# Optimization experiments

Measured on AMD Instinct MI355X. Metric: run time of the kernel, lower is better.

## Reference

```python
import jax, jax.numpy as jnp
import numpy as np

JITTER_EPS = 0.01  # router_jitter_noise


def sparsemixer_top2(scores, jitter_eps):
    # scores: [T, E]. Faithful port of PhiMoE sparsemixer (top_k == 2).
    E = scores.shape[-1]
    eye = jnp.arange(E)
    # ---- expert 1 ----
    max1 = jnp.max(scores, axis=-1, keepdims=True)
    ind1 = jnp.argmax(scores, axis=-1)                      # [T]
    factor1 = jnp.maximum(jnp.abs(scores), max1)            # scores.abs().clamp(min=max)
    mask1 = (max1 - scores) / factor1 > 2.0 * jitter_eps
    gates1 = jax.nn.softmax(jnp.where(mask1, -jnp.inf, scores), axis=-1)
    mult1 = jnp.take_along_axis(gates1, ind1[:, None], axis=-1)   # [T,1]
    # ---- expert 2: mask out first pick, repeat ----
    oh1 = eye[None, :] == ind1[:, None]
    masked_scores = jnp.where(oh1, -jnp.inf, scores)
    max2 = jnp.max(masked_scores, axis=-1, keepdims=True)
    ind2 = jnp.argmax(masked_scores, axis=-1)
    factor2 = jnp.maximum(jnp.abs(scores), max2)
    mask2 = (max2 - scores) / factor2 > 2.0 * jitter_eps
    gates2 = jax.nn.softmax(jnp.where(mask2, -jnp.inf, masked_scores), axis=-1)
    mult2 = jnp.take_along_axis(gates2, ind2[:, None], axis=-1)   # [T,1]
    topk_w = jnp.concatenate([mult1, mult2], axis=-1)       # [T,2]
    topk_ids = jnp.stack([ind1, ind2], axis=-1)             # [T,2]
    return topk_w, topk_ids


def setup_inputs() -> dict:
    key = jax.random.key(0)
    ks = jax.random.split(key, 5)
    B, S, D, F, E = 2, 2048, 1024, 2048, 8
    hidden_states = jax.random.normal(ks[0], (B, S, D), dtype=jnp.float32)
    gate_w = jax.random.normal(ks[1], (E, D), dtype=jnp.float32) * (D ** -0.5)
    w_gate = jax.random.normal(ks[2], (E, F, D), dtype=jnp.float32) * (D ** -0.5)
    w_up = jax.random.normal(ks[3], (E, F, D), dtype=jnp.float32) * (D ** -0.5)
    w_down = jax.random.normal(ks[4], (E, D, F), dtype=jnp.float32) * (F ** -0.5)
    return {"hidden_states": hidden_states, "gate_w": gate_w,
            "w_gate": w_gate, "w_up": w_up, "w_down": w_down}


def reference(hidden_states, gate_w, w_gate, w_up, w_down):
    B, S, D = hidden_states.shape
    E = gate_w.shape[0]
    x = hidden_states.reshape(-1, D)                         # [T,D]
    router_logits = x @ gate_w.T                             # [T,E]
    topk_w, topk_ids = sparsemixer_top2(router_logits, JITTER_EPS)
    # per-token combine weights over experts: [T,E]
    comb = jnp.sum(topk_w[:, :, None] *
                   (topk_ids[:, :, None] == jnp.arange(E)[None, None, :]).astype(topk_w.dtype),
                   axis=1)
    out = jnp.zeros_like(x)
    for e in range(E):  # small fixed expert count
        h = jax.nn.silu(x @ w_gate[e].T) * (x @ w_up[e].T)   # [T,F]
        out = out + comb[:, e:e + 1] * (h @ w_down[e].T)     # [T,D]
    return out.reshape(B, S, D), router_logits
```

## Files before the change

kernel.cpp:

```cpp
#include <hip/hip_runtime.h>
#include <stdint.h>

#define TOK    4096
#define DMODEL 1024
#define FDIM   2048
#define NEXP   8
#define MAXP   10240
#define MAXT   40
#define OUT_MAIN (TOK * DMODEL)

#define IDX_NT  24
#define IDX_TE  32
#define IDX_TR  112

#define OFF_META 0
#define OFF_TKW  33792
#define OFF_PTOK 66560
#define OFF_PW   107520
#define OFF_XG   148480
#define OFF_H    21120000
#define OFF_WGB  63063040
#define OFF_WUB  96617472
#define OFF_WDB  130171904
#define OFF_PV   OFF_WGB
#define OFF_RPOS 163726336
#define WS_NEED  163759104

typedef __attribute__((ext_vector_type(8)))  __bf16 bf16x8;
typedef __attribute__((ext_vector_type(8)))  unsigned short u16x8;
typedef __attribute__((ext_vector_type(4)))  unsigned short u16x4;
typedef __attribute__((ext_vector_type(16))) float f32x16;

__device__ __forceinline__ unsigned short f2bf(float f) {
  unsigned u = __builtin_bit_cast(unsigned, f);
  u += 0x7fffu + ((u >> 16) & 1u);
  return (unsigned short)(u >> 16);
}

__device__ __forceinline__ void async_load16(const void* g, void* l) {
  __builtin_amdgcn_global_load_lds(
      (__attribute__((address_space(1))) void*)g,
      (__attribute__((address_space(3))) void*)l, 16, 0, 0);
}

__device__ __forceinline__ bf16x8 ld_frag(const unsigned short* p) {
  return __builtin_bit_cast(bf16x8, *(const u16x8*)p);
}

__global__ void k_prep(const float* __restrict__ wg, const float* __restrict__ wu,
                       const float* __restrict__ wd, unsigned short* __restrict__ wgb,
                       unsigned short* __restrict__ wub, unsigned short* __restrict__ wdb,
                       const float* __restrict__ x, const float* __restrict__ gw,
                       float* __restrict__ logits, int pre) {
  int b = blockIdx.x;
  if (b < 24576) {
    if (!pre) return;
    const float* src; unsigned short* dst; int bb;
    if (b < 8192)       { src = wg; dst = wgb; bb = b; }
    else if (b < 16384) { src = wu; dst = wub; bb = b - 8192; }
    else                { src = wd; dst = wdb; bb = b - 16384; }
    size_t i = ((size_t)bb * 256 + threadIdx.x) * 8;
    float4 a = *(const float4*)(src + i);
    float4 c = *(const float4*)(src + i + 4);
    u16x8 v = {f2bf(a.x), f2bf(a.y), f2bf(a.z), f2bf(a.w),
               f2bf(c.x), f2bf(c.y), f2bf(c.z), f2bf(c.w)};
    *(u16x8*)(dst + i) = v;
    return;
  }
  int lane = threadIdx.x & 63;
  int t = (b - 24576) * 4 + (threadIdx.x >> 6);
  double acc[NEXP];
#pragma unroll
  for (int e = 0; e < NEXP; ++e) acc[e] = 0.0;
  const float* xp = x + (size_t)t * DMODEL;
  for (int i = 0; i < DMODEL / 64; ++i) {
    int d = i * 64 + lane;
    float xv = xp[d];
#pragma unroll
    for (int e = 0; e < NEXP; ++e) acc[e] += (double)xv * (double)gw[e * DMODEL + d];
  }
#pragma unroll
  for (int e = 0; e < NEXP; ++e) {
    double v = acc[e];
#pragma unroll
    for (int off = 32; off > 0; off >>= 1) v += __shfl_down(v, off, 64);
    if (lane == 0) logits[t * NEXP + e] = (float)v;
  }
}

__global__ __launch_bounds__(1024) void k_route2(
    const float* __restrict__ logits, int* __restrict__ meta,
    float* __restrict__ tk_w, int* __restrict__ ptok, float* __restrict__ pw,
    int* __restrict__ rpos) {
  __shared__ int cnt[NEXP], cur[NEXP], seg[NEXP];
  int tid = threadIdx.x;
  if (tid < NEXP) { cnt[tid] = 0; cur[tid] = 0; }
  for (int r = tid; r < MAXP; r += 1024) ptok[r] = -1;
  __syncthreads();
  int i1[4], i2[4]; float w1v[4], w2v[4];
#pragma unroll
  for (int j = 0; j < 4; ++j) {
    int t = tid + j * 1024;
    float s[NEXP];
#pragma unroll
    for (int e = 0; e < NEXP; ++e) s[e] = logits[t * NEXP + e];
    float max1 = s[0]; int ind1 = 0;
#pragma unroll
    for (int e = 1; e < NEXP; ++e) if (s[e] > max1) { max1 = s[e]; ind1 = e; }
    float sum1 = 0.f;
#pragma unroll
    for (int e = 0; e < NEXP; ++e) {
      float f = fmaxf(fabsf(s[e]), max1);
      if (!((max1 - s[e]) / f > 0.02f)) sum1 += expf(s[e] - max1);
    }
    float max2 = -3.4e38f; int ind2 = 0;
#pragma unroll
    for (int e = 0; e < NEXP; ++e) if (e != ind1 && s[e] > max2) { max2 = s[e]; ind2 = e; }
    float sum2 = 0.f;
#pragma unroll
    for (int e = 0; e < NEXP; ++e) {
      if (e == ind1) continue;
      float f = fmaxf(fabsf(s[e]), max2);
      if (!((max2 - s[e]) / f > 0.02f)) sum2 += expf(s[e] - max2);
    }
    i1[j] = ind1; i2[j] = ind2; w1v[j] = 1.f / sum1; w2v[j] = 1.f / sum2;
    atomicAdd(&cnt[ind1], 1);
    atomicAdd(&cnt[ind2], 1);
  }
  __syncthreads();
  if (tid == 0) {
    int off = 0, nt2 = 0;
    for (int e = 0; e < NEXP; ++e) {
      seg[e] = off;
      int tiles = (cnt[e] + 255) >> 8;
      for (int j = 0; j < tiles; ++j) {
        meta[IDX_TE + nt2] = e;
        meta[IDX_TR + nt2] = off + (j << 8);
        ++nt2;
      }
      off += tiles << 8;
    }
    meta[IDX_NT] = nt2;
  }
  __syncthreads();
#pragma unroll
  for (int j = 0; j < 4; ++j) {
    int t = tid + j * 1024;
    int e1 = i1[j];
    int p1 = atomicAdd(&cur[e1], 1);
    int r1 = seg[e1] + p1;
    ptok[r1] = t; pw[r1] = w1v[j]; rpos[2 * t] = r1; tk_w[2 * t] = w1v[j];
    int e2 = i2[j];
    int p2 = atomicAdd(&cur[e2], 1);
    int r2 = seg[e2] + p2;
    ptok[r2] = t; pw[r2] = w2v[j]; rpos[2 * t + 1] = r2; tk_w[2 * t + 1] = w2v[j];
  }
}

__global__ void k_gather(const float* __restrict__ x, const int* __restrict__ ptok,
                         unsigned short* __restrict__ xg) {
  int r = blockIdx.x;
  int t = ptok[r];
  int c = threadIdx.x << 2;
  unsigned short o0 = 0, o1 = 0, o2 = 0, o3 = 0;
  if (t >= 0) {
    float4 v = *(const float4*)(x + ((size_t)t << 10) + c);
    o0 = f2bf(v.x); o1 = f2bf(v.y); o2 = f2bf(v.z); o3 = f2bf(v.w);
  }
  u16x4 o = {o0, o1, o2, o3};
  *(u16x4*)(xg + ((size_t)r << 10) + c) = o;
}

template <bool PRE>
__global__ __launch_bounds__(512, 2) void k_gu(
    const unsigned short* __restrict__ xg,
    const float* __restrict__ wg32, const float* __restrict__ wu32,
    const unsigned short* __restrict__ wgb, const unsigned short* __restrict__ wub,
    unsigned short* __restrict__ h, const int* __restrict__ meta) {
  int p = blockIdx.x;
  int xcd = p & 7, slot = p >> 3;
  int bx = (slot / 40) * 8 + (slot & 7);
  int rt = xcd * 5 + ((slot % 40) >> 3);

  int nt = meta[IDX_NT];
  if (rt >= nt) return;
  int e = meta[IDX_TE + rt];
  int row0 = meta[IDX_TR + rt];
  int n0 = bx * 128;

  __shared__ __align__(16) unsigned short sA[2][16384];
  __shared__ __align__(16) unsigned short sBg[2][8192];
  __shared__ __align__(16) unsigned short sBu[2][8192];

  int tid = threadIdx.x, lane = tid & 63, w = tid >> 6;
  int wm = w & 1, wn = w >> 1;
  int l31 = lane & 31, lh = lane >> 5;

  f32x16 accg[4], accu[4];
#pragma unroll
  for (int m = 0; m < 4; ++m) {
#pragma unroll
    for (int r = 0; r < 16; ++r) { accg[m][r] = 0.f; accu[m][r] = 0.f; }
  }

  const unsigned short* Abase =
      xg + (size_t)(row0 + w * 32 + l31) * DMODEL + lh * 8;
  int cb0 = w * 2, cb1 = cb0 + 1;
  const unsigned short *G0, *G1, *U0, *U1;
  if constexpr (PRE) {
    const unsigned short* WgB = wgb + (size_t)e * FDIM * DMODEL;
    const unsigned short* WuB = wub + (size_t)e * FDIM * DMODEL;
    size_t o0 = (size_t)(n0 + ((cb0 >> 2) << 5) + l31) * DMODEL + ((cb0 & 3) << 4) + lh * 8;
    size_t o1 = (size_t)(n0 + ((cb1 >> 2) << 5) + l31) * DMODEL + ((cb1 & 3) << 4) + lh * 8;
    G0 = WgB + o0; G1 = WgB + o1; U0 = WuB + o0; U1 = WuB + o1;
  }
  const float* Wg = nullptr; const float* Wu = nullptr;
  if constexpr (!PRE) {
    Wg = wg32 + (size_t)e * FDIM * DMODEL;
    Wu = wu32 + (size_t)e * FDIM * DMODEL;
  }

  auto stage = [&](int buf, int ks) {
    int k0 = ks * 64;
    async_load16(Abase + k0,      &sA[buf][(w * 4 + 0) * 512]);
    async_load16(Abase + k0 + 16, &sA[buf][(w * 4 + 1) * 512]);
    async_load16(Abase + k0 + 32, &sA[buf][(w * 4 + 2) * 512]);
    async_load16(Abase + k0 + 48, &sA[buf][(w * 4 + 3) * 512]);
    if constexpr (PRE) {
      async_load16(G0 + k0, &sBg[buf][cb0 * 512]);
      async_load16(G1 + k0, &sBg[buf][cb1 * 512]);
      async_load16(U0 + k0, &sBu[buf][cb0 * 512]);
      async_load16(U1 + k0, &sBu[buf][cb1 * 512]);
    } else {
#pragma unroll
      for (int i2 = 0; i2 < 2; ++i2) {
        int tau = tid + 512 * i2;
        int c = tau >> 6, l = tau & 63;
        int nrow = n0 + ((c >> 2) << 5) + (l & 31);
        int kk = k0 + ((c & 3) << 4) + ((l >> 5) << 3);
        const float* sg = Wg + (size_t)nrow * DMODEL + kk;
        const float* su = Wu + (size_t)nrow * DMODEL + kk;
        float4 g0 = *(const float4*)sg;
        float4 g1 = *(const float4*)(sg + 4);
        float4 u0 = *(const float4*)su;
        float4 u1 = *(const float4*)(su + 4);
        u16x8 vg = {f2bf(g0.x), f2bf(g0.y), f2bf(g0.z), f2bf(g0.w),
                    f2bf(g1.x), f2bf(g1.y), f2bf(g1.z), f2bf(g1.w)};
        u16x8 vu = {f2bf(u0.x), f2bf(u0.y), f2bf(u0.z), f2bf(u0.w),
                    f2bf(u1.x), f2bf(u1.y), f2bf(u1.z), f2bf(u1.w)};
        *(u16x8*)&sBg[buf][c * 512 + l * 8] = vg;
        *(u16x8*)&sBu[buf][c * 512 + l * 8] = vu;
      }
    }
  };

  auto compute = [&](int buf) {
#pragma unroll
    for (int kq = 0; kq < 4; ++kq) {
      bf16x8 a0 = ld_frag(&sA[buf][((wm * 4 + 0) * 4 + kq) * 512 + lane * 8]);
      bf16x8 a1 = ld_frag(&sA[buf][((wm * 4 + 1) * 4 + kq) * 512 + lane * 8]);
      bf16x8 a2 = ld_frag(&sA[buf][((wm * 4 + 2) * 4 + kq) * 512 + lane * 8]);
      bf16x8 a3 = ld_frag(&sA[buf][((wm * 4 + 3) * 4 + kq) * 512 + lane * 8]);
      bf16x8 vg = ld_frag(&sBg[buf][(wn * 4 + kq) * 512 + lane * 8]);
      bf16x8 vu = ld_frag(&sBu[buf][(wn * 4 + kq) * 512 + lane * 8]);
      accg[0] = __builtin_amdgcn_mfma_f32_32x32x16_bf16(a0, vg, accg[0], 0, 0, 0);
      accg[1] = __builtin_amdgcn_mfma_f32_32x32x16_bf16(a1, vg, accg[1], 0, 0, 0);
      accg[2] = __builtin_amdgcn_mfma_f32_32x32x16_bf16(a2, vg, accg[2], 0, 0, 0);
      accg[3] = __builtin_amdgcn_mfma_f32_32x32x16_bf16(a3, vg, accg[3], 0, 0, 0);
      accu[0] = __builtin_amdgcn_mfma_f32_32x32x16_bf16(a0, vu, accu[0], 0, 0, 0);
      accu[1] = __builtin_amdgcn_mfma_f32_32x32x16_bf16(a1, vu, accu[1], 0, 0, 0);
      accu[2] = __builtin_amdgcn_mfma_f32_32x32x16_bf16(a2, vu, accu[2], 0, 0, 0);
      accu[3] = __builtin_amdgcn_mfma_f32_32x32x16_bf16(a3, vu, accu[3], 0, 0, 0);
    }
  };

  int cur = 0;
  stage(0, 0);
  if constexpr (PRE) {
#pragma unroll 2
    for (int ks = 0; ks < DMODEL / 64; ++ks) {
      if (ks + 1 < DMODEL / 64) {
        stage(cur ^ 1, ks + 1);
        asm volatile("s_waitcnt vmcnt(8)" ::: "memory");
      } else {
        asm volatile("s_waitcnt vmcnt(0)" ::: "memory");
      }
      __builtin_amdgcn_s_barrier();
      __builtin_amdgcn_s_setprio(1);
      compute(cur);
      __builtin_amdgcn_s_setprio(0);
      __builtin_amdgcn_s_barrier();
      cur ^= 1;
    }
  } else {
    __syncthreads();
    for (int ks = 0; ks < DMODEL / 64; ++ks) {
      if (ks + 1 < DMODEL / 64) stage(cur ^ 1, ks + 1);
      compute(cur);
      __syncthreads();
      cur ^= 1;
    }
  }

  int col = n0 + wn * 32 + l31;
#pragma unroll
  for (int m = 0; m < 4; ++m) {
#pragma unroll
    for (int r = 0; r < 16; ++r) {
      int lrow = wm * 128 + m * 32 + (r & 3) + ((r >> 2) << 3) + lh * 4;
      float gv = accg[m][r], uv = accu[m][r];
      float hv = gv * uv / (1.f + __expf(-gv));
      h[(size_t)(row0 + lrow) * FDIM + col] = f2bf(hv);
    }
  }
}

template <bool PRE>
__global__ __launch_bounds__(512, 2) void k_down(
    const unsigned short* __restrict__ h, const float* __restrict__ wd32,
    const unsigned short* __restrict__ wdb, float* __restrict__ out,
    float* __restrict__ pv, const int* __restrict__ meta,
    const int* __restrict__ ptok, const float* __restrict__ pw) {
  int p = blockIdx.x;
  int xcd = p & 7, slot = p >> 3;
  int bx = slot & 7;
  int rt = xcd * 5 + (slot >> 3);

  int nt = meta[IDX_NT];
  if (rt >= nt) return;
  int e = meta[IDX_TE + rt];
  int row0 = meta[IDX_TR + rt];
  int d0 = bx * 128;

  __shared__ __align__(16) unsigned short sA[2][16384];
  __shared__ __align__(16) unsigned short sB[2][8192];
  __shared__ int stok[256];
  __shared__ float sw_[256];

  int tid = threadIdx.x, lane = tid & 63, w = tid >> 6;
  int wm = w & 1, wn = w >> 1;
  int l31 = lane & 31, lh = lane >> 5;

  if constexpr (!PRE) {
    if (tid < 256) { stok[tid] = ptok[row0 + tid]; sw_[tid] = pw[row0 + tid]; }
  }

  f32x16 acc[4];
#pragma unroll
  for (int m = 0; m < 4; ++m) {
#pragma unroll
    for (int r = 0; r < 16; ++r) acc[m][r] = 0.f;
  }

  const unsigned short* Abase =
      h + (size_t)(row0 + w * 32 + l31) * FDIM + lh * 8;
  int cb0 = w * 2, cb1 = cb0 + 1;
  const unsigned short *D0, *D1;
  if constexpr (PRE) {
    const unsigned short* WdB = wdb + (size_t)e * DMODEL * FDIM;
    D0 = WdB + (size_t)(d0 + ((cb0 >> 2) << 5) + l31) * FDIM + ((cb0 & 3) << 4) + lh * 8;
    D1 = WdB + (size_t)(d0 + ((cb1 >> 2) << 5) + l31) * FDIM + ((cb1 & 3) << 4) + lh * 8;
  }
  const float* Wd = nullptr;
  if constexpr (!PRE) Wd = wd32 + (size_t)e * DMODEL * FDIM;

  auto stage = [&](int buf, int ks) {
    int k0 = ks * 64;
    async_load16(Abase + k0,      &sA[buf][(w * 4 + 0) * 512]);
    async_load16(Abase + k0 + 16, &sA[buf][(w * 4 + 1) * 512]);
    async_load16(Abase + k0 + 32, &sA[buf][(w * 4 + 2) * 512]);
    async_load16(Abase + k0 + 48, &sA[buf][(w * 4 + 3) * 512]);
    if constexpr (PRE) {
      async_load16(D0 + k0, &sB[buf][cb0 * 512]);
      async_load16(D1 + k0, &sB[buf][cb1 * 512]);
    } else {
#pragma unroll
      for (int i2 = 0; i2 < 2; ++i2) {
        int tau = tid + 512 * i2;
        int c = tau >> 6, l = tau & 63;
        int drow = d0 + ((c >> 2) << 5) + (l & 31);
        int kk = k0 + ((c & 3) << 4) + ((l >> 5) << 3);
        const float* sd = Wd + (size_t)drow * FDIM + kk;
        float4 b0 = *(const float4*)sd;
        float4 b1 = *(const float4*)(sd + 4);
        u16x8 vb = {f2bf(b0.x), f2bf(b0.y), f2bf(b0.z), f2bf(b0.w),
                    f2bf(b1.x), f2bf(b1.y), f2bf(b1.z), f2bf(b1.w)};
        *(u16x8*)&sB[buf][c * 512 + l * 8] = vb;
      }
    }
  };

  auto compute = [&](int buf) {
#pragma unroll
    for (int kq = 0; kq < 4; ++kq) {
      bf16x8 a0 = ld_frag(&sA[buf][((wm * 4 + 0) * 4 + kq) * 512 + lane * 8]);
      bf16x8 a1 = ld_frag(&sA[buf][((wm * 4 + 1) * 4 + kq) * 512 + lane * 8]);
      bf16x8 a2 = ld_frag(&sA[buf][((wm * 4 + 2) * 4 + kq) * 512 + lane * 8]);
      bf16x8 a3 = ld_frag(&sA[buf][((wm * 4 + 3) * 4 + kq) * 512 + lane * 8]);
      bf16x8 vb = ld_frag(&sB[buf][(wn * 4 + kq) * 512 + lane * 8]);
      acc[0] = __builtin_amdgcn_mfma_f32_32x32x16_bf16(a0, vb, acc[0], 0, 0, 0);
      acc[1] = __builtin_amdgcn_mfma_f32_32x32x16_bf16(a1, vb, acc[1], 0, 0, 0);
      acc[2] = __builtin_amdgcn_mfma_f32_32x32x16_bf16(a2, vb, acc[2], 0, 0, 0);
      acc[3] = __builtin_amdgcn_mfma_f32_32x32x16_bf16(a3, vb, acc[3], 0, 0, 0);
    }
  };

  int cur = 0;
  stage(0, 0);
  if constexpr (PRE) {
#pragma unroll 2
    for (int ks = 0; ks < FDIM / 64; ++ks) {
      if (ks + 1 < FDIM / 64) {
        stage(cur ^ 1, ks + 1);
        asm volatile("s_waitcnt vmcnt(6)" ::: "memory");
      } else {
        asm volatile("s_waitcnt vmcnt(0)" ::: "memory");
      }
      __builtin_amdgcn_s_barrier();
      __builtin_amdgcn_s_setprio(1);
      compute(cur);
      __builtin_amdgcn_s_setprio(0);
      __builtin_amdgcn_s_barrier();
      cur ^= 1;
    }
  } else {
    __syncthreads();
    for (int ks = 0; ks < FDIM / 64; ++ks) {
      if (ks + 1 < FDIM / 64) stage(cur ^ 1, ks + 1);
      compute(cur);
      __syncthreads();
      cur ^= 1;
    }
  }

  int col = d0 + wn * 32 + l31;
#pragma unroll
  for (int m = 0; m < 4; ++m) {
#pragma unroll
    for (int r = 0; r < 16; ++r) {
      int lrow = wm * 128 + m * 32 + (r & 3) + ((r >> 2) << 3) + lh * 4;
      if constexpr (PRE) {
        pv[(size_t)(row0 + lrow) * DMODEL + col] = acc[m][r];
      } else {
        int t = stok[lrow];
        if (t >= 0) atomicAdd(&out[(size_t)t * DMODEL + col], acc[m][r] * sw_[lrow]);
      }
    }
  }
}

__global__ void k_combine(const float* __restrict__ pv, const int* __restrict__ rpos,
                          const float* __restrict__ tkw, float* __restrict__ out) {
  int t = blockIdx.x;
  int r1 = rpos[2 * t], r2 = rpos[2 * t + 1];
  float w1 = tkw[2 * t], w2 = tkw[2 * t + 1];
  int c = threadIdx.x << 2;
  float4 a = *(const float4*)(pv + (size_t)r1 * DMODEL + c);
  float4 b = *(const float4*)(pv + (size_t)r2 * DMODEL + c);
  float4 o;
  o.x = w1 * a.x + w2 * b.x;
  o.y = w1 * a.y + w2 * b.y;
  o.z = w1 * a.z + w2 * b.z;
  o.w = w1 * a.w + w2 * b.w;
  *(float4*)(out + (size_t)t * DMODEL + c) = o;
}

extern "C" void kernel_launch(void* const* d_in, const int* in_sizes, int n_in,
                              void* d_out, int out_size, void* d_ws, size_t ws_size,
                              hipStream_t stream) {
  const float* x  = (const float*)d_in[0];
  const float* gw = (const float*)d_in[1];
  const float* wg = (const float*)d_in[2];
  const float* wu = (const float*)d_in[3];
  const float* wd = (const float*)d_in[4];
  float* out = (float*)d_out;
  float* logits = out + OUT_MAIN;

  char* wsb = (char*)d_ws;
  int* meta = (int*)(wsb + OFF_META);
  float* tk_w = (float*)(wsb + OFF_TKW);
  int* ptok = (int*)(wsb + OFF_PTOK);
  float* pw = (float*)(wsb + OFF_PW);
  unsigned short* xg = (unsigned short*)(wsb + OFF_XG);
  unsigned short* h = (unsigned short*)(wsb + OFF_H);
  unsigned short* wgb = (unsigned short*)(wsb + OFF_WGB);
  unsigned short* wub = (unsigned short*)(wsb + OFF_WUB);
  unsigned short* wdb = (unsigned short*)(wsb + OFF_WDB);
  float* pv = (float*)(wsb + OFF_PV);
  int* rpos = (int*)(wsb + OFF_RPOS);

  bool pre = ws_size >= (size_t)WS_NEED;
  if (!pre) hipMemsetAsync(out, 0, (size_t)OUT_MAIN * sizeof(float), stream);

  k_prep<<<25600, 256, 0, stream>>>(wg, wu, wd, wgb, wub, wdb, x, gw, logits, (int)pre);
  k_route2<<<1, 1024, 0, stream>>>(logits, meta, tk_w, ptok, pw, rpos);
  k_gather<<<MAXP, 256, 0, stream>>>(x, ptok, xg);
  if (pre) {
    k_gu<true><<<(FDIM / 128) * MAXT, 512, 0, stream>>>(xg, wg, wu, wgb, wub, h, meta);
    k_down<true><<<(DMODEL / 128) * MAXT, 512, 0, stream>>>(h, wd, wdb, out, pv, meta, ptok, pw);
    k_combine<<<TOK, 256, 0, stream>>>(pv, rpos, tk_w, out);
  } else {
    k_gu<false><<<(FDIM / 128) * MAXT, 512, 0, stream>>>(xg, wg, wu, wgb, wub, h, meta);
    k_down<false><<<(DMODEL / 128) * MAXT, 512, 0, stream>>>(h, wd, wdb, out, pv, meta, ptok, pw);
  }
}
```

Measured before the change: 542.2 us.

## Pre-tile weights, gathered activations and intermediate into fragment-contiguous blocked layout

Weight conversion, token gather and the gate/up epilogue now write bf16 data in a blocked layout where each 64-lane 16-byte async load reads one contiguous 1KB chunk. The goal is fully coalesced global->LDS transfers in the gate/up and down GEMMs instead of strided row reads. The cost is extra index math, a prep launch that goes from 25600 to 41984 blocks with half the threads idle in the gate/up part, and scattered 2-byte stores of h in the epilogue. The fp32 fallback path (no-pre) still expects row-major A, and that consistency is unclear.

After: 501.4 us. -7.5%, faster.

```diff
diff --git a/kernel.cpp b/kernel.cpp
--- a/kernel.cpp
+++ b/kernel.cpp
@@ -53,22 +53,45 @@
                        const float* __restrict__ x, const float* __restrict__ gw,
                        float* __restrict__ logits, int pre) {
   int b = blockIdx.x;
-  if (b < 24576) {
+  if (b < 40960) {
     if (!pre) return;
-    const float* src; unsigned short* dst; int bb;
-    if (b < 8192)       { src = wg; dst = wgb; bb = b; }
-    else if (b < 16384) { src = wu; dst = wub; bb = b - 8192; }
-    else                { src = wd; dst = wdb; bb = b - 16384; }
-    size_t i = ((size_t)bb * 256 + threadIdx.x) * 8;
-    float4 a = *(const float4*)(src + i);
-    float4 c = *(const float4*)(src + i + 4);
-    u16x8 v = {f2bf(a.x), f2bf(a.y), f2bf(a.z), f2bf(a.w),
-               f2bf(c.x), f2bf(c.y), f2bf(c.z), f2bf(c.w)};
-    *(u16x8*)(dst + i) = v;
+    if (b < 32768) {
+      const float* src = (b < 16384) ? wg : wu;
+      unsigned short* dst = (b < 16384) ? wgb : wub;
+      int gr = b & 16383;
+      int e = gr >> 11, n = gr & 2047;
+      int bx = n >> 7, nsub = (n >> 5) & 3, l31 = n & 31;
+      int p = threadIdx.x;
+      if (p < 128) {
+        int ks = p >> 3, kq = (p >> 1) & 3, lh = p & 1;
+        const float* s = src + (size_t)gr * 1024 + p * 8;
+        float4 a = *(const float4*)s;
+        float4 c = *(const float4*)(s + 4);
+        u16x8 v = {f2bf(a.x), f2bf(a.y), f2bf(a.z), f2bf(a.w),
+                   f2bf(c.x), f2bf(c.y), f2bf(c.z), f2bf(c.w)};
+        size_t off = ((((size_t)(e * 16 + bx) * 16 + ks) * 16) + nsub * 4 + kq) * 512 +
+                     (size_t)(l31 + 32 * lh) * 8;
+        *(u16x8*)(dst + off) = v;
+      }
+    } else {
+      int gr = b - 32768;
+      int e = gr >> 10, d = gr & 1023;
+      int bx = d >> 7, nsub = (d >> 5) & 3, l31 = d & 31;
+      int p = threadIdx.x;
+      int ks = p >> 3, kq = (p >> 1) & 3, lh = p & 1;
+      const float* s = wd + (size_t)gr * 2048 + p * 8;
+      float4 a = *(const float4*)s;
+      float4 c = *(const float4*)(s + 4);
+      u16x8 v = {f2bf(a.x), f2bf(a.y), f2bf(a.z), f2bf(a.w),
+                 f2bf(c.x), f2bf(c.y), f2bf(c.z), f2bf(c.w)};
+      size_t off = ((((size_t)(e * 8 + bx) * 32 + ks) * 16) + nsub * 4 + kq) * 512 +
+                   (size_t)(l31 + 32 * lh) * 8;
+      *(u16x8*)(wdb + off) = v;
+    }
     return;
   }
   int lane = threadIdx.x & 63;
-  int t = (b - 24576) * 4 + (threadIdx.x >> 6);
+  int t = (b - 40960) * 4 + (threadIdx.x >> 6);
   double acc[NEXP];
 #pragma unroll
   for (int e = 0; e < NEXP; ++e) acc[e] = 0.0;
@@ -159,16 +182,22 @@
 
 __global__ void k_gather(const float* __restrict__ x, const int* __restrict__ ptok,
                          unsigned short* __restrict__ xg) {
-  int r = blockIdx.x;
-  int t = ptok[r];
-  int c = threadIdx.x << 2;
-  unsigned short o0 = 0, o1 = 0, o2 = 0, o3 = 0;
+  int rr = blockIdx.x;
+  int t = ptok[rr];
+  int rt = rr >> 8, msub = (rr >> 5) & 7, l31 = rr & 31;
+  int p = threadIdx.x;
+  int ks = p >> 3, kq = (p >> 1) & 3, lh = p & 1;
+  u16x8 v = {0, 0, 0, 0, 0, 0, 0, 0};
   if (t >= 0) {
-    float4 v = *(const float4*)(x + ((size_t)t << 10) + c);
-    o0 = f2bf(v.x); o1 = f2bf(v.y); o2 = f2bf(v.z); o3 = f2bf(v.w);
-  }
-  u16x4 o = {o0, o1, o2, o3};
-  *(u16x4*)(xg + ((size_t)r << 10) + c) = o;
+    const float* s = x + ((size_t)t << 10) + p * 8;
+    float4 a = *(const float4*)s;
+    float4 c = *(const float4*)(s + 4);
+    v = (u16x8){f2bf(a.x), f2bf(a.y), f2bf(a.z), f2bf(a.w),
+                f2bf(c.x), f2bf(c.y), f2bf(c.z), f2bf(c.w)};
+  }
+  size_t off = (((size_t)(rt * 16 + ks) * 32) + msub * 4 + kq) * 512 +
+               (size_t)(l31 + 32 * lh) * 8;
+  *(u16x8*)(xg + off) = v;
 }
 
 template <bool PRE>
@@ -203,16 +232,14 @@
     for (int r = 0; r < 16; ++r) { accg[m][r] = 0.f; accu[m][r] = 0.f; }
   }
 
-  const unsigned short* Abase =
-      xg + (size_t)(row0 + w * 32 + l31) * DMODEL + lh * 8;
+  const unsigned short* A0 =
+      xg + (((size_t)rt * 16) * 32 + w * 4) * 512 + (size_t)lane * 8;
   int cb0 = w * 2, cb1 = cb0 + 1;
-  const unsigned short *G0, *G1, *U0, *U1;
+  const unsigned short *Bg0, *Bu0;
   if constexpr (PRE) {
-    const unsigned short* WgB = wgb + (size_t)e * FDIM * DMODEL;
-    const unsigned short* WuB = wub + (size_t)e * FDIM * DMODEL;
-    size_t o0 = (size_t)(n0 + ((cb0 >> 2) << 5) + l31) * DMODEL + ((cb0 & 3) << 4) + lh * 8;
-    size_t o1 = (size_t)(n0 + ((cb1 >> 2) << 5) + l31) * DMODEL + ((cb1 & 3) << 4) + lh * 8;
-    G0 = WgB + o0; G1 = WgB + o1; U0 = WuB + o0; U1 = WuB + o1;
+    size_t pb = (((size_t)(e * 16 + bx) * 16) * 16 + cb0) * 512 + (size_t)lane * 8;
+    Bg0 = wgb + pb;
+    Bu0 = wub + pb;
   }
   const float* Wg = nullptr; const float* Wu = nullptr;
   if constexpr (!PRE) {
@@ -221,17 +248,19 @@
   }
 
   auto stage = [&](int buf, int ks) {
-    int k0 = ks * 64;
-    async_load16(Abase + k0,      &sA[buf][(w * 4 + 0) * 512]);
-    async_load16(Abase + k0 + 16, &sA[buf][(w * 4 + 1) * 512]);
-    async_load16(Abase + k0 + 32, &sA[buf][(w * 4 + 2) * 512]);
-    async_load16(Abase + k0 + 48, &sA[buf][(w * 4 + 3) * 512]);
+    size_t ao = (size_t)ks * 16384;
+    async_load16(A0 + ao,        &sA[buf][(w * 4 + 0) * 512]);
+    async_load16(A0 + ao + 512,  &sA[buf][(w * 4 + 1) * 512]);
+    async_load16(A0 + ao + 1024, &sA[buf][(w * 4 + 2) * 512]);
+    async_load16(A0 + ao + 1536, &sA[buf][(w * 4 + 3) * 512]);
     if constexpr (PRE) {
-      async_load16(G0 + k0, &sBg[buf][cb0 * 512]);
-      async_load16(G1 + k0, &sBg[buf][cb1 * 512]);
-      async_load16(U0 + k0, &sBu[buf][cb0 * 512]);
-      async_load16(U1 + k0, &sBu[buf][cb1 * 512]);
+      size_t bo = (size_t)ks * 8192;
+      async_load16(Bg0 + bo,       &sBg[buf][cb0 * 512]);
+      async_load16(Bg0 + bo + 512, &sBg[buf][cb1 * 512]);
+      async_load16(Bu0 + bo,       &sBu[buf][cb0 * 512]);
+      async_load16(Bu0 + bo + 512, &sBu[buf][cb1 * 512]);
     } else {
+      int k0 = ks * 64;
 #pragma unroll
       for (int i2 = 0; i2 < 2; ++i2) {
         int tau = tid + 512 * i2;
@@ -302,15 +331,19 @@
     }
   }
 
-  int col = n0 + wn * 32 + l31;
+  int ks2 = bx * 2 + (wn >> 1);
+  int kq2 = ((wn & 1) << 1) + (l31 >> 4);
+  int lh2 = (l31 >> 3) & 1;
+  int jj = l31 & 7;
 #pragma unroll
   for (int m = 0; m < 4; ++m) {
+    size_t cbase = ((size_t)(rt * 32 + ks2) * 32 + (wm * 4 + m) * 4 + kq2) * 512;
 #pragma unroll
     for (int r = 0; r < 16; ++r) {
-      int lrow = wm * 128 + m * 32 + (r & 3) + ((r >> 2) << 3) + lh * 4;
+      int l31p = (r & 3) + ((r >> 2) << 3) + lh * 4;
       float gv = accg[m][r], uv = accu[m][r];
       float hv = gv * uv / (1.f + __expf(-gv));
-      h[(size_t)(row0 + lrow) * FDIM + col] = f2bf(hv);
+      h[cbase + (size_t)(l31p + 32 * lh2) * 8 + jj] = f2bf(hv);
     }
   }
 }
@@ -352,28 +385,28 @@
     for (int r = 0; r < 16; ++r) acc[m][r] = 0.f;
   }
 
-  const unsigned short* Abase =
-      h + (size_t)(row0 + w * 32 + l31) * FDIM + lh * 8;
+  const unsigned short* A0 =
+      h + (((size_t)rt * 32) * 32 + w * 4) * 512 + (size_t)lane * 8;
   int cb0 = w * 2, cb1 = cb0 + 1;
-  const unsigned short *D0, *D1;
+  const unsigned short* B0;
   if constexpr (PRE) {
-    const unsigned short* WdB = wdb + (size_t)e * DMODEL * FDIM;
-    D0 = WdB + (size_t)(d0 + ((cb0 >> 2) << 5) + l31) * FDIM + ((cb0 & 3) << 4) + lh * 8;
-    D1 = WdB + (size_t)(d0 + ((cb1 >> 2) << 5) + l31) * FDIM + ((cb1 & 3) << 4) + lh * 8;
+    B0 = wdb + (((size_t)(e * 8 + bx) * 32) * 16 + cb0) * 512 + (size_t)lane * 8;
   }
   const float* Wd = nullptr;
   if constexpr (!PRE) Wd = wd32 + (size_t)e * DMODEL * FDIM;
 
   auto stage = [&](int buf, int ks) {
-    int k0 = ks * 64;
-    async_load16(Abase + k0,      &sA[buf][(w * 4 + 0) * 512]);
-    async_load16(Abase + k0 + 16, &sA[buf][(w * 4 + 1) * 512]);
-    async_load16(Abase + k0 + 32, &sA[buf][(w * 4 + 2) * 512]);
-    async_load16(Abase + k0 + 48, &sA[buf][(w * 4 + 3) * 512]);
+    size_t ao = (size_t)ks * 16384;
+    async_load16(A0 + ao,        &sA[buf][(w * 4 + 0) * 512]);
+    async_load16(A0 + ao + 512,  &sA[buf][(w * 4 + 1) * 512]);
+    async_load16(A0 + ao + 1024, &sA[buf][(w * 4 + 2) * 512]);
+    async_load16(A0 + ao + 1536, &sA[buf][(w * 4 + 3) * 512]);
     if constexpr (PRE) {
-      async_load16(D0 + k0, &sB[buf][cb0 * 512]);
-      async_load16(D1 + k0, &sB[buf][cb1 * 512]);
+      size_t bo = (size_t)ks * 8192;
+      async_load16(B0 + bo,       &sB[buf][cb0 * 512]);
+      async_load16(B0 + bo + 512, &sB[buf][cb1 * 512]);
     } else {
+      int k0 = ks * 64;
 #pragma unroll
       for (int i2 = 0; i2 < 2; ++i2) {
         int tau = tid + 512 * i2;
@@ -492,9 +525,9 @@
   bool pre = ws_size >= (size_t)WS_NEED;
   if (!pre) hipMemsetAsync(out, 0, (size_t)OUT_MAIN * sizeof(float), stream);
 
-  k_prep<<<25600, 256, 0, stream>>>(wg, wu, wd, wgb, wub, wdb, x, gw, logits, (int)pre);
+  k_prep<<<41984, 256, 0, stream>>>(wg, wu, wd, wgb, wub, wdb, x, gw, logits, (int)pre);
   k_route2<<<1, 1024, 0, stream>>>(logits, meta, tk_w, ptok, pw, rpos);
-  k_gather<<<MAXP, 256, 0, stream>>>(x, ptok, xg);
+  k_gather<<<MAXP, 128, 0, stream>>>(x, ptok, xg);
   if (pre) {
     k_gu<true><<<(FDIM / 128) * MAXT, 512, 0, stream>>>(xg, wg, wu, wgb, wub, h, meta);
     k_down<true><<<(DMODEL / 128) * MAXT, 512, 0, stream>>>(h, wd, wdb, out, pv, meta, ptok, pw);
```
